# Performance work log

Measured on AMD Instinct MI355X. Metric: run time of the kernel, lower is better.

## Reference

```python
import jax, jax.numpy as jnp
import numpy as np

D_MODEL = 768
N_HEADS = 12
NUM_EXPERTS = 4
TOP_K = 2
SPAN_LEN = 64
GATE_HIDDEN = 128


def setup_inputs() -> dict:
    key = jax.random.key(0)
    ks = jax.random.split(key, 14)
    B, T, C, E = 4, 4096, D_MODEL, NUM_EXPERTS
    s = 0.02
    return {
        "hidden_states": jax.random.normal(ks[0], (B, T, C), jnp.float32),
        "Wq": jax.random.normal(ks[1], (E, C, C), jnp.float32) * s,
        "bq": jnp.zeros((E, C), jnp.float32),
        "Wk": jax.random.normal(ks[2], (E, C, C), jnp.float32) * s,
        "bk": jnp.zeros((E, C), jnp.float32),
        "Wv": jax.random.normal(ks[3], (E, C, C), jnp.float32) * s,
        "bv": jnp.zeros((E, C), jnp.float32),
        "gW1": jax.random.normal(ks[4], (GATE_HIDDEN, C), jnp.float32) * s,
        "gb1": jnp.zeros((GATE_HIDDEN,), jnp.float32),
        "gW2": jax.random.normal(ks[5], (E, GATE_HIDDEN), jnp.float32) * s,
        "gb2": jnp.zeros((E,), jnp.float32),
        "Wo": jax.random.normal(ks[6], (C, C), jnp.float32) * s,
        "bo": jnp.zeros((C,), jnp.float32),
    }


def _moe_proj(w, x, W, b):
    # per-expert projection then gate-weighted sum over experts
    # x: (B,N,S,C), W: (E,O,C), w: (B,N,E)
    proj = jnp.einsum("bnsc,eoc->ebnso", x, W)          # (E,B,N,S,C)
    out = jnp.einsum("bne,ebnso->bnso", w, proj)
    out = out + jnp.einsum("bne,eo->bno", w, b)[:, :, None, :]
    return out


def reference(hidden_states, Wq, bq, Wk, bk, Wv, bv, gW1, gb1, gW2, gb2, Wo, bo):
    B, T, C = hidden_states.shape
    S, H, E, K = SPAN_LEN, N_HEADS, NUM_EXPERTS, TOP_K
    Dh = C // H
    N = T // S  # T is a multiple of span_len -> no padding, all-ones masks
    x = hidden_states.reshape(B, N, S, C)

    # gating: mean-pool per span -> MLP -> top-k softmax scattered to E slots
    pooled = x.mean(axis=2)                                  # (B,N,C)
    h = jax.nn.relu(pooled @ gW1.T + gb1)
    logits = h @ gW2.T + gb2                                 # (B,N,E)
    vals, idx = jax.lax.top_k(logits, K)
    sm = jax.nn.softmax(vals, axis=-1)                       # (B,N,K)
    w = jnp.sum(jax.nn.one_hot(idx, E, dtype=sm.dtype) * sm[..., None], axis=-2)  # (B,N,E)
    entropy = -jnp.mean(jnp.sum(w * jnp.log(jnp.clip(w, 1e-9)), axis=-1))

    # gate-weighted expert QKV projections
    q = _moe_proj(w, x, Wq, bq).reshape(B, N, S, H, Dh)
    k = _moe_proj(w, x, Wk, bk).reshape(B, N, S, H, Dh)
    v = _moe_proj(w, x, Wv, bv).reshape(B, N, S, H, Dh)

    # per-span attention (mask is all ones; dropout in eval mode)
    scores = jnp.einsum("bnshd,bnthd->bnhst", q, k) / jnp.sqrt(jnp.float32(Dh))
    attn = jax.nn.softmax(scores, axis=-1)
    out = jnp.einsum("bnhst,bnthd->bnshd", attn, v).reshape(B, T, C)
    out = out @ Wo.T + bo
    return out, entropy
```

## Files before the change

### kernel.cpp

```cpp
#include <hip/hip_runtime.h>
#include <hip/hip_bf16.h>
#include <hip/hip_fp16.h>

typedef _Float16 f16;
typedef _Float16 f16x8 __attribute__((ext_vector_type(8)));
typedef _Float16 f16x4 __attribute__((ext_vector_type(4)));
typedef float f32x4 __attribute__((ext_vector_type(4)));

constexpr int B = 4;
constexpr int T = 4096;
constexpr int C = 768;
constexpr int NH = 12;
constexpr int DH = 64;
constexpr int E = 4;
constexpr int SPAN = 64;
constexpr int N = T / SPAN;
constexpr int BN = B * N;
constexpr int GH = 128;
constexpr int BTC = B * T * C;

constexpr int U_WE = E * C * C / 8;
constexpr int U_WO = C * C / 8;
constexpr int U_WTOT = 3 * U_WE + U_WO;

#define LGKM_BARRIER()                                      \
    do {                                                    \
        asm volatile("s_waitcnt lgkmcnt(0)" ::: "memory");  \
        __builtin_amdgcn_s_barrier();                       \
        __builtin_amdgcn_sched_barrier(0);                  \
    } while (0)

__global__ __launch_bounds__(768) void cvt_x_pool(
    const float* __restrict__ x, f16* __restrict__ x16,
    float* __restrict__ pooled) {
    int span = blockIdx.x;
    int tid = threadIdx.x;
    int u = tid % 96, rg = tid / 96;
    __shared__ float part[8][C];

    const float* xb = x + (size_t)span * SPAN * C;
    f16* xo = x16 + (size_t)span * SPAN * C;
    float a8[8] = {};
    #pragma unroll
    for (int j = 0; j < 8; ++j) {
        int r = rg * 8 + j;
        const float4* s = (const float4*)(xb + (size_t)r * C + u * 8);
        float4 A = s[0], Bv = s[1];
        f16x8 o;
        o[0] = (f16)A.x;  o[1] = (f16)A.y;  o[2] = (f16)A.z;  o[3] = (f16)A.w;
        o[4] = (f16)Bv.x; o[5] = (f16)Bv.y; o[6] = (f16)Bv.z; o[7] = (f16)Bv.w;
        *(f16x8*)(xo + (size_t)r * C + u * 8) = o;
        a8[0] += A.x;  a8[1] += A.y;  a8[2] += A.z;  a8[3] += A.w;
        a8[4] += Bv.x; a8[5] += Bv.y; a8[6] += Bv.z; a8[7] += Bv.w;
    }
    #pragma unroll
    for (int j = 0; j < 8; ++j) part[rg][u * 8 + j] = a8[j];
    __syncthreads();
    float s = 0.f;
    #pragma unroll
    for (int g = 0; g < 8; ++g) s += part[g][tid];
    pooled[(size_t)span * C + tid] = s * (1.f / 64.f);
}

__global__ void cvt_w(const float* __restrict__ Wq, const float* __restrict__ Wk,
                      const float* __restrict__ Wv, const float* __restrict__ Wo,
                      f16* __restrict__ Wq16, f16* __restrict__ Wk16,
                      f16* __restrict__ Wv16, f16* __restrict__ Wo16) {
    int i = blockIdx.x * blockDim.x + threadIdx.x;
    int stride = gridDim.x * blockDim.x;
    for (; i < U_WTOT; i += stride) {
        const float* src; f16* dst; int u;
        if (i < U_WE)               { src = Wq; dst = Wq16; u = i; }
        else if (i < 2 * U_WE)      { src = Wk; dst = Wk16; u = i - U_WE; }
        else if (i < 3 * U_WE)      { src = Wv; dst = Wv16; u = i - 2 * U_WE; }
        else                        { src = Wo; dst = Wo16; u = i - 3 * U_WE; }
        float4 a = ((const float4*)src)[2 * u];
        float4 b = ((const float4*)src)[2 * u + 1];
        f16x8 o;
        o[0] = (f16)a.x; o[1] = (f16)a.y; o[2] = (f16)a.z; o[3] = (f16)a.w;
        o[4] = (f16)b.x; o[5] = (f16)b.y; o[6] = (f16)b.z; o[7] = (f16)b.w;
        ((f16x8*)dst)[u] = o;
    }
}

__global__ __launch_bounds__(128) void gate_mlp(
    const float* __restrict__ pooled,
    const float* __restrict__ gW1, const float* __restrict__ gb1,
    const float* __restrict__ gW2, const float* __restrict__ gb2,
    int* __restrict__ eidx, float* __restrict__ ewts,
    float* __restrict__ ent_partial) {
    int span = blockIdx.x;
    int tid = threadIdx.x;
    __shared__ float pl[C];
    __shared__ float h[GH];
    __shared__ float logits[E];

    for (int c = tid; c < C; c += 128) pl[c] = pooled[(size_t)span * C + c];
    __syncthreads();

    {
        float acc = gb1[tid];
        const float* wrow = gW1 + (size_t)tid * C;
        #pragma unroll 8
        for (int c = 0; c < C; ++c) acc += pl[c] * wrow[c];
        h[tid] = acc > 0.f ? acc : 0.f;
    }
    __syncthreads();

    if (tid < E) {
        float acc = gb2[tid];
        const float* wrow = gW2 + (size_t)tid * GH;
        #pragma unroll 8
        for (int j = 0; j < GH; ++j) acc += h[j] * wrow[j];
        logits[tid] = acc;
    }
    __syncthreads();

    if (tid == 0) {
        int i0 = 0; float v0 = logits[0];
        for (int e = 1; e < E; ++e) { if (logits[e] > v0) { v0 = logits[e]; i0 = e; } }
        int i1 = -1; float v1 = -3.0e38f;
        for (int e = 0; e < E; ++e) { if (e != i0 && logits[e] > v1) { v1 = logits[e]; i1 = e; } }
        float bq_ = expf(v1 - v0);
        float s = 1.f + bq_;
        float sm0 = 1.f / s;
        float sm1 = bq_ / s;
        eidx[span * 2 + 0] = i0;
        eidx[span * 2 + 1] = i1;
        ewts[span * 2 + 0] = sm0;
        ewts[span * 2 + 1] = sm1;
        float p0 = fmaxf(sm0, 1e-9f), p1 = fmaxf(sm1, 1e-9f);
        ent_partial[span] = sm0 * logf(p0) + sm1 * logf(p1);
    }
}

__global__ void entropy_kernel(const float* __restrict__ ent_partial, float* __restrict__ out_ent) {
    __shared__ float sh[256];
    int tid = threadIdx.x;
    sh[tid] = ent_partial[tid];
    __syncthreads();
    for (int s = 128; s > 0; s >>= 1) {
        if (tid < s) sh[tid] += sh[tid + s];
        __syncthreads();
    }
    if (tid == 0) *out_ent = -sh[0] * (1.0f / (float)BN);
}

__global__ __launch_bounds__(256) void qkv_mfma(
    const f16* __restrict__ xh,
    const f16* __restrict__ Wq16, const float* __restrict__ bq,
    const f16* __restrict__ Wk16, const float* __restrict__ bk,
    const f16* __restrict__ Wv16, const float* __restrict__ bv,
    const int* __restrict__ eidx, const float* __restrict__ ewts,
    f16* __restrict__ q16, f16* __restrict__ k16, f16* __restrict__ vt)
{
    int span  = blockIdx.x;
    int otile = blockIdx.y;
    int proj  = blockIdx.z;

    const f16* W; const float* bias; f16* out;
    if (proj == 0)      { W = Wq16; bias = bq; out = q16; }
    else if (proj == 1) { W = Wk16; bias = bk; out = k16; }
    else                { W = Wv16; bias = bv; out = vt; }

    int e0 = eidx[span * 2 + 0], e1 = eidx[span * 2 + 1];
    float w0 = ewts[span * 2 + 0], w1 = ewts[span * 2 + 1];
    f16 w0h = (f16)w0, w1h = (f16)w1;

    __shared__ f16x8 xs_u[64 * 8];
    __shared__ f16x8 ws_u[256 * 8];

    const f16x8* xu  = (const f16x8*)(xh + (size_t)span * 64 * C);
    const f16x8* Wu0 = (const f16x8*)(W + ((size_t)e0 * C + otile * 256) * (size_t)C);
    const f16x8* Wu1 = (const f16x8*)(W + ((size_t)e1 * C + otile * 256) * (size_t)C);

    int tid = threadIdx.x;
    int lane = tid & 63, wv = tid >> 6;
    int lr = lane & 15, lg = lane >> 4;

    f32x4 acc[4][4] = {};

    f16x8 xr[2], w0r[8], w1r[8];
    #pragma unroll
    for (int i = 0; i < 2; ++i) {
        int id = tid + i * 256;
        xr[i] = xu[(id >> 3) * 96 + (id & 7)];
    }
    #pragma unroll
    for (int i = 0; i < 8; ++i) {
        int id = tid + i * 256;
        w0r[i] = Wu0[(size_t)(id >> 3) * 96 + (id & 7)];
        w1r[i] = Wu1[(size_t)(id >> 3) * 96 + (id & 7)];
    }

    for (int kc8 = 0; kc8 < 96; kc8 += 8) {
        #pragma unroll
        for (int i = 0; i < 2; ++i) {
            int id = tid + i * 256;
            int r = id >> 3, u = id & 7;
            xs_u[r * 8 + (u ^ (r & 7))] = xr[i];
        }
        #pragma unroll
        for (int i = 0; i < 8; ++i) {
            int id = tid + i * 256;
            int r = id >> 3, u = id & 7;
            ws_u[r * 8 + (u ^ (r & 7))] = w0r[i] * w0h + w1r[i] * w1h;
        }

        if (kc8 < 88) {
            int kn = kc8 + 8;
            #pragma unroll
            for (int i = 0; i < 2; ++i) {
                int id = tid + i * 256;
                xr[i] = xu[(id >> 3) * 96 + kn + (id & 7)];
            }
            #pragma unroll
            for (int i = 0; i < 8; ++i) {
                int id = tid + i * 256;
                w0r[i] = Wu0[(size_t)(id >> 3) * 96 + kn + (id & 7)];
                w1r[i] = Wu1[(size_t)(id >> 3) * 96 + kn + (id & 7)];
            }
        }

        LGKM_BARRIER();

        #pragma unroll
        for (int kk = 0; kk < 2; ++kk) {
            int ub = kk * 4 + lg;
            f16x8 afrag[4], bfrag[4];
            #pragma unroll
            for (int m = 0; m < 4; ++m) {
                int r = m * 16 + lr;
                afrag[m] = xs_u[r * 8 + (ub ^ (r & 7))];
            }
            #pragma unroll
            for (int n = 0; n < 4; ++n) {
                int r = wv * 64 + n * 16 + lr;
                bfrag[n] = ws_u[r * 8 + (ub ^ (r & 7))];
            }
            #pragma unroll
            for (int m = 0; m < 4; ++m)
                #pragma unroll
                for (int n = 0; n < 4; ++n)
                    acc[m][n] = __builtin_amdgcn_mfma_f32_16x16x32_f16(afrag[m], bfrag[n], acc[m][n], 0, 0, 0);
        }

        LGKM_BARRIER();
    }

    if (proj == 2) {
        f16* vtb = out + (size_t)span * C * 64;
        #pragma unroll
        for (int n = 0; n < 4; ++n) {
            int col = otile * 256 + wv * 64 + n * 16 + lr;
            float be = w0 * bias[(size_t)e0 * C + col] + w1 * bias[(size_t)e1 * C + col];
            #pragma unroll
            for (int m = 0; m < 4; ++m) {
                f16x4 pk;
                #pragma unroll
                for (int r = 0; r < 4; ++r) pk[r] = (f16)(acc[m][n][r] + be);
                *(f16x4*)&vtb[(size_t)col * 64 + m * 16 + lg * 4] = pk;
            }
        }
    } else {
        f16* outb = out + (size_t)span * 64 * C;
        #pragma unroll
        for (int n = 0; n < 4; ++n) {
            int col = otile * 256 + wv * 64 + n * 16 + lr;
            float be = w0 * bias[(size_t)e0 * C + col] + w1 * bias[(size_t)e1 * C + col];
            #pragma unroll
            for (int m = 0; m < 4; ++m) {
                #pragma unroll
                for (int r = 0; r < 4; ++r) {
                    int row = m * 16 + lg * 4 + r;
                    outb[(size_t)row * C + col] = (f16)(acc[m][n][r] + be);
                }
            }
        }
    }
}

__global__ __launch_bounds__(256) void attn_mfma(
    const f16* __restrict__ q16, const f16* __restrict__ k16,
    const f16* __restrict__ vt, f16* __restrict__ a16)
{
    int h = blockIdx.x, span = blockIdx.y;
    __shared__ __align__(16) f16 Klds[64 * 72];
    __shared__ __align__(16) f16 Vlds[64 * 72];
    __shared__ __align__(16) f16 Plds[64 * 72];

    int tid = threadIdx.x;
    int lane = tid & 63, mt = tid >> 6;
    int lr = lane & 15, lg = lane >> 4;

    const f16x8* ku = (const f16x8*)k16;
    const f16x8* vu = (const f16x8*)vt;
    #pragma unroll
    for (int i = 0; i < 2; ++i) {
        int id = tid + i * 256;
        int r = id >> 3, u = id & 7;
        *(f16x8*)&Klds[r * 72 + u * 8] = ku[(size_t)span * 6144 + (size_t)r * 96 + h * 8 + u];
        *(f16x8*)&Vlds[r * 72 + u * 8] = vu[(size_t)span * 6144 + (size_t)(h * 64 + r) * 8 + u];
    }
    const f16x8* qu = (const f16x8*)q16;
    f16x8 qa[2];
    #pragma unroll
    for (int kk = 0; kk < 2; ++kk)
        qa[kk] = qu[(size_t)span * 6144 + (size_t)(mt * 16 + lr) * 96 + h * 8 + kk * 4 + lg];

    LGKM_BARRIER();

    f32x4 accs[4] = {};
    #pragma unroll
    for (int nt = 0; nt < 4; ++nt) {
        #pragma unroll
        for (int kk = 0; kk < 2; ++kk) {
            f16x8 kb = *(const f16x8*)&Klds[(nt * 16 + lr) * 72 + kk * 32 + lg * 8];
            accs[nt] = __builtin_amdgcn_mfma_f32_16x16x32_f16(qa[kk], kb, accs[nt], 0, 0, 0);
        }
    }

    #pragma unroll
    for (int nt = 0; nt < 4; ++nt) accs[nt] *= 0.125f;
    f32x4 m4;
    #pragma unroll
    for (int r = 0; r < 4; ++r)
        m4[r] = fmaxf(fmaxf(accs[0][r], accs[1][r]), fmaxf(accs[2][r], accs[3][r]));
    #pragma unroll
    for (int st = 1; st < 16; st <<= 1) {
        #pragma unroll
        for (int r = 0; r < 4; ++r) m4[r] = fmaxf(m4[r], __shfl_xor(m4[r], st));
    }
    f32x4 ps[4];
    f32x4 sum4 = {0.f, 0.f, 0.f, 0.f};
    #pragma unroll
    for (int nt = 0; nt < 4; ++nt)
        #pragma unroll
        for (int r = 0; r < 4; ++r) {
            ps[nt][r] = __expf(accs[nt][r] - m4[r]);
            sum4[r] += ps[nt][r];
        }
    #pragma unroll
    for (int st = 1; st < 16; st <<= 1) {
        #pragma unroll
        for (int r = 0; r < 4; ++r) sum4[r] += __shfl_xor(sum4[r], st);
    }
    f32x4 inv4;
    #pragma unroll
    for (int r = 0; r < 4; ++r) inv4[r] = 1.0f / sum4[r];

    #pragma unroll
    for (int nt = 0; nt < 4; ++nt)
        #pragma unroll
        for (int r = 0; r < 4; ++r)
            Plds[(mt * 16 + lg * 4 + r) * 72 + nt * 16 + lr] = (f16)ps[nt][r];

    LGKM_BARRIER();

    f16x8 pa[2];
    #pragma unroll
    for (int kkt = 0; kkt < 2; ++kkt)
        pa[kkt] = *(const f16x8*)&Plds[(mt * 16 + lr) * 72 + kkt * 32 + lg * 8];
    f32x4 acco[4] = {};
    #pragma unroll
    for (int nt = 0; nt < 4; ++nt) {
        #pragma unroll
        for (int kkt = 0; kkt < 2; ++kkt) {
            f16x8 vb = *(const f16x8*)&Vlds[(nt * 16 + lr) * 72 + kkt * 32 + lg * 8];
            acco[nt] = __builtin_amdgcn_mfma_f32_16x16x32_f16(pa[kkt], vb, acco[nt], 0, 0, 0);
        }
    }

    #pragma unroll
    for (int nt = 0; nt < 4; ++nt)
        #pragma unroll
        for (int r = 0; r < 4; ++r)
            Klds[(mt * 16 + lg * 4 + r) * 72 + nt * 16 + lr] = (f16)(acco[nt][r] * inv4[r]);

    LGKM_BARRIER();

    int row = mt * 16 + (lane >> 2);
    int u2 = (lane & 3) * 2;
    f16x8 o0 = *(const f16x8*)&Klds[row * 72 + u2 * 8];
    f16x8 o1 = *(const f16x8*)&Klds[row * 72 + u2 * 8 + 8];
    f16x8* au = (f16x8*)a16;
    au[(size_t)span * 6144 + (size_t)row * 96 + h * 8 + u2]     = o0;
    au[(size_t)span * 6144 + (size_t)row * 96 + h * 8 + u2 + 1] = o1;
}

__global__ __launch_bounds__(512) void outproj_mfma(
    const f16* __restrict__ ah, const f16* __restrict__ Wo16,
    const float* __restrict__ bo, float* __restrict__ Y)
{
    int rt = blockIdx.x;
    int otile = blockIdx.y;

    __shared__ f16x8 as_u[128 * 8];
    __shared__ f16x8 ws_u[256 * 8];

    const f16x8* au  = (const f16x8*)(ah + (size_t)rt * 128 * C);
    const f16x8* Wou = (const f16x8*)(Wo16 + (size_t)otile * 256 * C);

    int tid = threadIdx.x;
    int lane = tid & 63, wv = tid >> 6;
    int lr = lane & 15, lg = lane >> 4;
    int wm = (wv >> 2) * 64;
    int wn = (wv & 3) * 64;

    f32x4 acc[4][4] = {};

    f16x8 ar_[2], wr_[4];
    #pragma unroll
    for (int i = 0; i < 2; ++i) {
        int id = tid + i * 512;
        ar_[i] = au[(size_t)(id >> 3) * 96 + (id & 7)];
    }
    #pragma unroll
    for (int i = 0; i < 4; ++i) {
        int id = tid + i * 512;
        wr_[i] = Wou[(size_t)(id >> 3) * 96 + (id & 7)];
    }

    for (int kc8 = 0; kc8 < 96; kc8 += 8) {
        #pragma unroll
        for (int i = 0; i < 2; ++i) {
            int id = tid + i * 512;
            int r = id >> 3, u = id & 7;
            as_u[r * 8 + (u ^ (r & 7))] = ar_[i];
        }
        #pragma unroll
        for (int i = 0; i < 4; ++i) {
            int id = tid + i * 512;
            int r = id >> 3, u = id & 7;
            ws_u[r * 8 + (u ^ (r & 7))] = wr_[i];
        }

        if (kc8 < 88) {
            int kn = kc8 + 8;
            #pragma unroll
            for (int i = 0; i < 2; ++i) {
                int id = tid + i * 512;
                ar_[i] = au[(size_t)(id >> 3) * 96 + kn + (id & 7)];
            }
            #pragma unroll
            for (int i = 0; i < 4; ++i) {
                int id = tid + i * 512;
                wr_[i] = Wou[(size_t)(id >> 3) * 96 + kn + (id & 7)];
            }
        }

        LGKM_BARRIER();

        #pragma unroll
        for (int kk = 0; kk < 2; ++kk) {
            int ub = kk * 4 + lg;
            f16x8 afrag[4], bfrag[4];
            #pragma unroll
            for (int m = 0; m < 4; ++m) {
                int r = wm + m * 16 + lr;
                afrag[m] = as_u[r * 8 + (ub ^ (r & 7))];
            }
            #pragma unroll
            for (int n = 0; n < 4; ++n) {
                int r = wn + n * 16 + lr;
                bfrag[n] = ws_u[r * 8 + (ub ^ (r & 7))];
            }
            #pragma unroll
            for (int m = 0; m < 4; ++m)
                #pragma unroll
                for (int n = 0; n < 4; ++n)
                    acc[m][n] = __builtin_amdgcn_mfma_f32_16x16x32_f16(afrag[m], bfrag[n], acc[m][n], 0, 0, 0);
        }

        LGKM_BARRIER();
    }

    #pragma unroll
    for (int n = 0; n < 4; ++n) {
        int col = otile * 256 + wn + n * 16 + lr;
        float be = bo[col];
        #pragma unroll
        for (int m = 0; m < 4; ++m) {
            #pragma unroll
            for (int r = 0; r < 4; ++r) {
                int row = rt * 128 + wm + m * 16 + lg * 4 + r;
                Y[(size_t)row * C + col] = acc[m][n][r] + be;
            }
        }
    }
}

extern "C" void kernel_launch(void* const* d_in, const int* in_sizes, int n_in,
                              void* d_out, int out_size, void* d_ws, size_t ws_size,
                              hipStream_t stream) {
    const float* x   = (const float*)d_in[0];
    const float* Wq  = (const float*)d_in[1];
    const float* bq  = (const float*)d_in[2];
    const float* Wk  = (const float*)d_in[3];
    const float* bk  = (const float*)d_in[4];
    const float* Wv  = (const float*)d_in[5];
    const float* bv  = (const float*)d_in[6];
    const float* gW1 = (const float*)d_in[7];
    const float* gb1 = (const float*)d_in[8];
    const float* gW2 = (const float*)d_in[9];
    const float* gb2 = (const float*)d_in[10];
    const float* Wo  = (const float*)d_in[11];
    const float* bo  = (const float*)d_in[12];

    float* out = (float*)d_out;

    char* ws = (char*)d_ws;
    const size_t h_btc = (size_t)BTC * sizeof(f16);
    f16* x16  = (f16*)(ws);
    f16* q16  = (f16*)(ws + 1 * h_btc);
    f16* k16  = (f16*)(ws + 2 * h_btc);
    f16* vt16 = (f16*)(ws + 3 * h_btc);
    f16* a16  = (f16*)(ws + 4 * h_btc);
    size_t off = 5 * h_btc;
    const size_t wsz = (size_t)E * C * C * sizeof(f16);
    f16* Wq16 = (f16*)(ws + off); off += wsz;
    f16* Wk16 = (f16*)(ws + off); off += wsz;
    f16* Wv16 = (f16*)(ws + off); off += wsz;
    f16* Wo16 = (f16*)(ws + off); off += (size_t)C * C * sizeof(f16);
    int*   eidx = (int*)(ws + off); off += 2048;
    float* ewts = (float*)(ws + off); off += 2048;
    float* entp = (float*)(ws + off); off += 1024;
    float* pooled = (float*)(ws + off); off += (size_t)BN * C * sizeof(float);

    cvt_x_pool<<<dim3(BN), dim3(768), 0, stream>>>(x, x16, pooled);
    cvt_w<<<dim3(1024), dim3(256), 0, stream>>>(Wq, Wk, Wv, Wo,
                                                Wq16, Wk16, Wv16, Wo16);
    gate_mlp<<<dim3(BN), dim3(128), 0, stream>>>(pooled, gW1, gb1, gW2, gb2,
                                                 eidx, ewts, entp);
    entropy_kernel<<<dim3(1), dim3(256), 0, stream>>>(entp, out + BTC);

    qkv_mfma<<<dim3(BN, 3, 3), dim3(256), 0, stream>>>(x16, Wq16, bq, Wk16, bk, Wv16, bv,
                                                       eidx, ewts, q16, k16, vt16);
    attn_mfma<<<dim3(NH, BN), dim3(256), 0, stream>>>(q16, k16, vt16, a16);
    outproj_mfma<<<dim3(128, 3), dim3(512), 0, stream>>>(a16, Wo16, bo, out);
}
```

Baseline: 213.2 us.

## Pre-swizzle x and expert weights into MFMA fragment order, drop LDS staging

The conversion kernels now write the fp16 activations and expert QKV weights in an MFMA-fragment-major layout, so each lane's fragment is a contiguous 16-byte load. The QKV GEMM then reads fragments straight from global memory into registers, mixes the two experts' weights in registers, and runs MFMAs without LDS staging or barriers. Occupancy is hinted with launch_bounds(256,3). The aim is to remove LDS traffic and synchronisation. The cost is that every wave reloads the shared x fragments and weight tiles from global/L2, with no block-level reuse, and global latency must now be hidden by unrolling and occupancy.

```diff
diff --git a/kernel.cpp b/kernel.cpp
--- a/kernel.cpp
+++ b/kernel.cpp
@@ -39,7 +39,8 @@
     __shared__ float part[8][C];
 
     const float* xb = x + (size_t)span * SPAN * C;
-    f16* xo = x16 + (size_t)span * SPAN * C;
+    f16x8* xo = (f16x8*)x16 + (size_t)span * 6144;
+    int kt = u >> 2, lg = u & 3;
     float a8[8] = {};
     #pragma unroll
     for (int j = 0; j < 8; ++j) {
@@ -49,7 +50,8 @@
         f16x8 o;
         o[0] = (f16)A.x;  o[1] = (f16)A.y;  o[2] = (f16)A.z;  o[3] = (f16)A.w;
         o[4] = (f16)Bv.x; o[5] = (f16)Bv.y; o[6] = (f16)Bv.z; o[7] = (f16)Bv.w;
-        *(f16x8*)(xo + (size_t)r * C + u * 8) = o;
+        int m = r >> 4, lr = r & 15;
+        xo[(kt * 4 + m) * 64 + lg * 16 + lr] = o;
         a8[0] += A.x;  a8[1] += A.y;  a8[2] += A.z;  a8[3] += A.w;
         a8[4] += Bv.x; a8[5] += Bv.y; a8[6] += Bv.z; a8[7] += Bv.w;
     }
@@ -70,16 +72,27 @@
     int stride = gridDim.x * blockDim.x;
     for (; i < U_WTOT; i += stride) {
         const float* src; f16* dst; int u;
+        bool frag = true;
         if (i < U_WE)               { src = Wq; dst = Wq16; u = i; }
         else if (i < 2 * U_WE)      { src = Wk; dst = Wk16; u = i - U_WE; }
         else if (i < 3 * U_WE)      { src = Wv; dst = Wv16; u = i - 2 * U_WE; }
-        else                        { src = Wo; dst = Wo16; u = i - 3 * U_WE; }
+        else                        { src = Wo; dst = Wo16; u = i - 3 * U_WE; frag = false; }
         float4 a = ((const float4*)src)[2 * u];
         float4 b = ((const float4*)src)[2 * u + 1];
         f16x8 o;
         o[0] = (f16)a.x; o[1] = (f16)a.y; o[2] = (f16)a.z; o[3] = (f16)a.w;
         o[4] = (f16)b.x; o[5] = (f16)b.y; o[6] = (f16)b.z; o[7] = (f16)b.w;
-        ((f16x8*)dst)[u] = o;
+        if (frag) {
+            int e   = u / (C * C / 8);
+            int rem = u - e * (C * C / 8);
+            int orow = rem / 96;
+            int ku   = rem - orow * 96;
+            int cb = orow >> 6, nn = (orow >> 4) & 3, lr = orow & 15;
+            int kt = ku >> 2, lg = ku & 3;
+            ((f16x8*)dst)[(size_t)(e * 12 + cb) * 6144 + (kt * 4 + nn) * 64 + lg * 16 + lr] = o;
+        } else {
+            ((f16x8*)dst)[u] = o;
+        }
     }
 }
 
@@ -146,7 +159,7 @@
     if (tid == 0) *out_ent = -sh[0] * (1.0f / (float)BN);
 }
 
-__global__ __launch_bounds__(256) void qkv_mfma(
+__global__ __launch_bounds__(256, 3) void qkv_mfma(
     const f16* __restrict__ xh,
     const f16* __restrict__ Wq16, const float* __restrict__ bq,
     const f16* __restrict__ Wk16, const float* __restrict__ bk,
@@ -167,92 +180,40 @@
     float w0 = ewts[span * 2 + 0], w1 = ewts[span * 2 + 1];
     f16 w0h = (f16)w0, w1h = (f16)w1;
 
-    __shared__ f16x8 xs_u[64 * 8];
-    __shared__ f16x8 ws_u[256 * 8];
-
-    const f16x8* xu  = (const f16x8*)(xh + (size_t)span * 64 * C);
-    const f16x8* Wu0 = (const f16x8*)(W + ((size_t)e0 * C + otile * 256) * (size_t)C);
-    const f16x8* Wu1 = (const f16x8*)(W + ((size_t)e1 * C + otile * 256) * (size_t)C);
-
     int tid = threadIdx.x;
     int lane = tid & 63, wv = tid >> 6;
     int lr = lane & 15, lg = lane >> 4;
+    int cb = otile * 4 + wv;
+
+    const f16x8* xu  = (const f16x8*)xh + (size_t)span * 6144 + lane;
+    const f16x8* wu0 = (const f16x8*)W + ((size_t)e0 * 12 + cb) * 6144 + lane;
+    const f16x8* wu1 = (const f16x8*)W + ((size_t)e1 * 12 + cb) * 6144 + lane;
 
     f32x4 acc[4][4] = {};
 
-    f16x8 xr[2], w0r[8], w1r[8];
-    #pragma unroll
-    for (int i = 0; i < 2; ++i) {
-        int id = tid + i * 256;
-        xr[i] = xu[(id >> 3) * 96 + (id & 7)];
-    }
-    #pragma unroll
-    for (int i = 0; i < 8; ++i) {
-        int id = tid + i * 256;
-        w0r[i] = Wu0[(size_t)(id >> 3) * 96 + (id & 7)];
-        w1r[i] = Wu1[(size_t)(id >> 3) * 96 + (id & 7)];
-    }
-
-    for (int kc8 = 0; kc8 < 96; kc8 += 8) {
-        #pragma unroll
-        for (int i = 0; i < 2; ++i) {
-            int id = tid + i * 256;
-            int r = id >> 3, u = id & 7;
-            xs_u[r * 8 + (u ^ (r & 7))] = xr[i];
-        }
-        #pragma unroll
-        for (int i = 0; i < 8; ++i) {
-            int id = tid + i * 256;
-            int r = id >> 3, u = id & 7;
-            ws_u[r * 8 + (u ^ (r & 7))] = w0r[i] * w0h + w1r[i] * w1h;
-        }
-
-        if (kc8 < 88) {
-            int kn = kc8 + 8;
-            #pragma unroll
-            for (int i = 0; i < 2; ++i) {
-                int id = tid + i * 256;
-                xr[i] = xu[(id >> 3) * 96 + kn + (id & 7)];
-            }
-            #pragma unroll
-            for (int i = 0; i < 8; ++i) {
-                int id = tid + i * 256;
-                w0r[i] = Wu0[(size_t)(id >> 3) * 96 + kn + (id & 7)];
-                w1r[i] = Wu1[(size_t)(id >> 3) * 96 + kn + (id & 7)];
-            }
-        }
-
-        LGKM_BARRIER();
-
-        #pragma unroll
-        for (int kk = 0; kk < 2; ++kk) {
-            int ub = kk * 4 + lg;
-            f16x8 afrag[4], bfrag[4];
-            #pragma unroll
-            for (int m = 0; m < 4; ++m) {
-                int r = m * 16 + lr;
-                afrag[m] = xs_u[r * 8 + (ub ^ (r & 7))];
-            }
-            #pragma unroll
-            for (int n = 0; n < 4; ++n) {
-                int r = wv * 64 + n * 16 + lr;
-                bfrag[n] = ws_u[r * 8 + (ub ^ (r & 7))];
-            }
-            #pragma unroll
-            for (int m = 0; m < 4; ++m)
-                #pragma unroll
-                for (int n = 0; n < 4; ++n)
-                    acc[m][n] = __builtin_amdgcn_mfma_f32_16x16x32_f16(afrag[m], bfrag[n], acc[m][n], 0, 0, 0);
-        }
-
-        LGKM_BARRIER();
+    #pragma unroll 4
+    for (int kt = 0; kt < 24; ++kt) {
+        f16x8 af[4], bf[4];
+        #pragma unroll
+        for (int m = 0; m < 4; ++m) af[m] = xu[(kt * 4 + m) * 64];
+        #pragma unroll
+        for (int n = 0; n < 4; ++n) {
+            f16x8 b0 = wu0[(kt * 4 + n) * 64];
+            f16x8 b1 = wu1[(kt * 4 + n) * 64];
+            bf[n] = b0 * w0h + b1 * w1h;
+        }
+        #pragma unroll
+        for (int m = 0; m < 4; ++m)
+            #pragma unroll
+            for (int n = 0; n < 4; ++n)
+                acc[m][n] = __builtin_amdgcn_mfma_f32_16x16x32_f16(af[m], bf[n], acc[m][n], 0, 0, 0);
     }
 
     if (proj == 2) {
         f16* vtb = out + (size_t)span * C * 64;
         #pragma unroll
         for (int n = 0; n < 4; ++n) {
-            int col = otile * 256 + wv * 64 + n * 16 + lr;
+            int col = cb * 64 + n * 16 + lr;
             float be = w0 * bias[(size_t)e0 * C + col] + w1 * bias[(size_t)e1 * C + col];
             #pragma unroll
             for (int m = 0; m < 4; ++m) {
@@ -266,7 +227,7 @@
         f16* outb = out + (size_t)span * 64 * C;
         #pragma unroll
         for (int n = 0; n < 4; ++n) {
-            int col = otile * 256 + wv * 64 + n * 16 + lr;
+            int col = cb * 64 + n * 16 + lr;
             float be = w0 * bias[(size_t)e0 * C + col] + w1 * bias[(size_t)e1 * C + col];
             #pragma unroll
             for (int m = 0; m < 4; ++m) {
```

After: 239.4 us. +12.3%, slower.
